# Kernel optimization log

Hardware: AMD Instinct MI355X
Metric: run time of the kernel (lower is better)

The kernel has to match this reference:

```python
import jax, jax.numpy as jnp
import numpy as np

NEG_SLOPE = 0.01  # torch nn.LeakyReLU default


def setup_inputs() -> dict:
    key = jax.random.key(0)
    k1, k2, k3 = jax.random.split(key, 3)
    B, H, D, L = 4, 8, 64, 2048
    q = jax.random.normal(k1, (B, H, D, L), dtype=jnp.float32)
    k = jax.random.normal(k2, (B, H, D, L), dtype=jnp.float32)
    v = jax.random.normal(k3, (B, H, D, L), dtype=jnp.float32)
    return {"q": q, "k": k, "v": v}


def reference(q, k, v):
    # q, k, v: [B, H, D, L] (note: feature dim BEFORE length, as in the torch module)
    d_tensor = q.shape[2]
    scale = 1.0 / np.sqrt(d_tensor).astype(np.float32)
    # scores = LeakyReLU(q^T k / sqrt(d)) : [B, H, Lq, Lk]
    scores = jnp.einsum('bhdq,bhdk->bhqk', q, k) * scale
    scores = jax.nn.leaky_relu(scores, negative_slope=NEG_SLOPE)
    psi = jax.nn.softmax(scores, axis=-1)
    # out = (psi @ v^T)^T : [B, H, D, Lq]
    out = jnp.einsum('bhqk,bhdk->bhdq', psi, v)
    return out
```

## Files before the change

kernel.cpp:

```cpp
#include <hip/hip_runtime.h>
#include <math.h>

#define DD 64
#define LL 2048
#define HEADS 32
#define TQ 128
#define TK 64
#define NTHREADS 512
#define QSCALE 0.18033688011112042f

typedef __bf16 bf16_t;
typedef __bf16 bf16x8 __attribute__((ext_vector_type(8)));
typedef float f32x16 __attribute__((ext_vector_type(16)));

__global__ __launch_bounds__(256)
void prep_bf16(const float* __restrict__ q, const float* __restrict__ k,
               const float* __restrict__ v, bf16_t* __restrict__ qt,
               bf16_t* __restrict__ kt, bf16_t* __restrict__ vb) {
  __shared__ float ld[64][65];
  const int t = threadIdx.x;
  const int which = blockIdx.z;
  const int head = blockIdx.y;
  const int l0 = blockIdx.x * 64;
  const size_t hoff = (size_t)head * DD * LL;
  if (which == 2) {
    const float* src = v + hoff;
    bf16_t* dst = vb + hoff;
    const int lp = (t & 31) * 2;
    const int db = (t >> 5) * 8;
    for (int i = 0; i < 8; ++i) {
      int d = db + i;
      float2 x = *(const float2*)(src + (size_t)d * LL + l0 + lp);
      union { bf16_t b[2]; unsigned u; } pk;
      pk.b[0] = (bf16_t)x.x;
      pk.b[1] = (bf16_t)x.y;
      *(unsigned*)(dst + (size_t)d * LL + l0 + lp) = pk.u;
    }
  } else {
    const float* src = (which == 0) ? (q + hoff) : (k + hoff);
    bf16_t* dst = (which == 0) ? (qt + hoff) : (kt + hoff);
    const float scale = (which == 0) ? QSCALE : 1.0f;
    const int l = t & 63;
    const int db = (t >> 6) * 16;
    for (int i = 0; i < 16; ++i) {
      int d = db + i;
      ld[l][d] = src[(size_t)d * LL + l0 + l] * scale;
    }
    __syncthreads();
    const int dp = (t & 31) * 2;
    const int lb = (t >> 5) * 8;
    for (int i = 0; i < 8; ++i) {
      int lw = lb + i;
      union { bf16_t b[2]; unsigned u; } pk;
      pk.b[0] = (bf16_t)ld[lw][dp];
      pk.b[1] = (bf16_t)ld[lw][dp + 1];
      *(unsigned*)(dst + (size_t)(l0 + lw) * DD + dp) = pk.u;
    }
  }
}

struct __align__(16) SMemA2 {
  bf16_t Qs[TQ][72];
  bf16_t Ks[2][TK][72];
  bf16_t Vs[2][DD][72];
};
union __align__(16) SMemU2 {
  SMemA2 a;
  float Oe[TQ][65];
};

__global__ __launch_bounds__(NTHREADS, 4)
void attn_flash_bf16_v2(const bf16_t* __restrict__ qt, const bf16_t* __restrict__ kt,
                        const bf16_t* __restrict__ vb, float* __restrict__ out) {
  __shared__ SMemU2 sm;
  __shared__ float rs1[TQ];
  const int tid  = threadIdx.x;
  const int w    = tid >> 6;
  const int lane = tid & 63;
  const int l31  = lane & 31;
  const int hh   = lane >> 5;
  const int strip = w & 3;
  const int half  = w >> 2;
  const int wbase = strip * 32;
  const int lkh   = half * 32;
  const int head = blockIdx.y;
  const int q0   = blockIdx.x * TQ;
  const size_t hoff = (size_t)head * DD * LL;
  const bf16_t* qp = qt + hoff;
  const bf16_t* kp = kt + hoff;
  const bf16_t* vp = vb + hoff;

  for (int g = 0; g < 2; ++g) {
    int c  = tid + NTHREADS * g;
    int lq = c >> 3;
    int d0 = (c & 7) * 8;
    bf16x8 x = *(const bf16x8*)(qp + (size_t)(q0 + lq) * DD + d0);
    *(bf16x8*)&sm.a.Qs[lq][d0] = x;
  }

  const int srow = tid >> 3;
  const int scol = (tid & 7) * 8;

  bf16x8 kreg = *(const bf16x8*)(kp + (size_t)srow * DD + scol);
  bf16x8 vreg = *(const bf16x8*)(vp + (size_t)srow * LL + scol);

  __syncthreads();
  bf16x8 bq[4];
  for (int kk = 0; kk < 4; ++kk)
    bq[kk] = *(const bf16x8*)&sm.a.Qs[wbase + l31][kk * 16 + 8 * hh];

  f32x16 oacc[2];
  for (int dt = 0; dt < 2; ++dt)
    for (int r = 0; r < 16; ++r) oacc[dt][r] = 0.f;
  float rsum = 0.f;

  for (int t = 0; t < LL / TK; ++t) {
    const int cur = t & 1;
    *(bf16x8*)&sm.a.Ks[cur][srow][scol] = kreg;
    *(bf16x8*)&sm.a.Vs[cur][srow][scol] = vreg;
    __syncthreads();

    if (t + 1 < LL / TK) {
      const int lk0n = (t + 1) * TK;
      kreg = *(const bf16x8*)(kp + (size_t)(lk0n + srow) * DD + scol);
      vreg = *(const bf16x8*)(vp + (size_t)srow * LL + lk0n + scol);
    }

    f32x16 st;
    for (int r = 0; r < 16; ++r) st[r] = 0.f;
    __builtin_amdgcn_s_setprio(1);
    for (int kk = 0; kk < 4; ++kk) {
      bf16x8 ak = *(const bf16x8*)&sm.a.Ks[cur][lkh + l31][kk * 16 + 8 * hh];
      st = __builtin_amdgcn_mfma_f32_32x32x16_bf16(ak, bq[kk], st, 0, 0, 0);
    }
    __builtin_amdgcn_s_setprio(0);

    unsigned pb[8];
    for (int r = 0; r < 16; ++r) {
      float s = st[r];
      s = fmaxf(s, 0.01f * s);
      float p = __builtin_amdgcn_exp2f(s);
      rsum += p;
      st[r] = p;
    }
    for (int qq = 0; qq < 8; ++qq) {
      union { bf16_t b[2]; unsigned u; } pk;
      pk.b[0] = (bf16_t)st[2 * qq];
      pk.b[1] = (bf16_t)st[2 * qq + 1];
      pb[qq] = pk.u;
    }

    for (int kk2 = 0; kk2 < 2; ++kk2) {
      unsigned l0 = pb[4 * kk2 + 0], l1 = pb[4 * kk2 + 1];
      unsigned l2 = pb[4 * kk2 + 2], l3 = pb[4 * kk2 + 3];
      unsigned s0 = hh ? l0 : l2;
      unsigned s1 = hh ? l1 : l3;
      unsigned f0 = (unsigned)__shfl_xor((int)s0, 32);
      unsigned f1 = (unsigned)__shfl_xor((int)s1, 32);
      union { unsigned u[4]; bf16x8 v; } ap;
      ap.u[0] = hh ? f0 : l0;
      ap.u[1] = hh ? f1 : l1;
      ap.u[2] = hh ? l2 : f0;
      ap.u[3] = hh ? l3 : f1;
      const int lkb = lkh + kk2 * 16 + 8 * hh;
      __builtin_amdgcn_s_setprio(1);
      for (int dt = 0; dt < 2; ++dt) {
        bf16x8 bv = *(const bf16x8*)&sm.a.Vs[cur][dt * 32 + l31][lkb];
        oacc[dt] = __builtin_amdgcn_mfma_f32_32x32x16_bf16(ap.v, bv, oacc[dt], 0, 0, 0);
      }
      __builtin_amdgcn_s_setprio(0);
    }
  }

  float rtot = rsum + __shfl_xor(rsum, 32);
  __syncthreads();
  if (half == 1) {
    rs1[wbase + l31] = rtot;
    for (int r = 0; r < 16; ++r) {
      int row = (r & 3) + 8 * (r >> 2) + 4 * hh;
      for (int dt = 0; dt < 2; ++dt)
        sm.Oe[wbase + row][dt * 32 + l31] = oacc[dt][r];
    }
  }
  __syncthreads();
  if (half == 0) {
    float tot = rtot + rs1[wbase + l31];
    rs1[wbase + l31] = 1.0f / tot;
    float inv[16];
    for (int r = 0; r < 16; ++r) {
      int row = (r & 3) + 8 * (r >> 2) + 4 * hh;
      inv[r] = rs1[wbase + row];
    }
    for (int r = 0; r < 16; ++r) {
      int row = (r & 3) + 8 * (r >> 2) + 4 * hh;
      for (int dt = 0; dt < 2; ++dt) {
        int col = dt * 32 + l31;
        sm.Oe[wbase + row][col] = (oacc[dt][r] + sm.Oe[wbase + row][col]) * inv[r];
      }
    }
  }
  __syncthreads();
  float* op = out + hoff + q0;
  for (int i = 0; i < 16; ++i) {
    int idx = tid + NTHREADS * i;
    int d   = idx >> 7;
    int lq  = idx & 127;
    op[(size_t)d * LL + lq] = sm.Oe[lq][d];
  }
}

struct __align__(16) SMemA {
  bf16_t Qs[TQ][72];
  bf16_t Ks[TK][72];
  bf16_t Vs[DD][72];
};
union __align__(16) SMemU {
  SMemA a;
  float Oe[TQ][65];
};

__global__ __launch_bounds__(NTHREADS, 4)
void attn_flash_bf16(const float* __restrict__ q, const float* __restrict__ k,
                     const float* __restrict__ v, float* __restrict__ out) {
  __shared__ SMemU sm;
  __shared__ float rs1[TQ];
  const int tid  = threadIdx.x;
  const int w    = tid >> 6;
  const int lane = tid & 63;
  const int l31  = lane & 31;
  const int hh   = lane >> 5;
  const int strip = w & 3;
  const int half  = w >> 2;
  const int wbase = strip * 32;
  const int lkh   = half * 32;
  const int head = blockIdx.y;
  const int q0   = blockIdx.x * TQ;
  const size_t hoff = (size_t)head * DD * LL;
  const float* qp = q + hoff;
  const float* kp = k + hoff;
  const float* vp = v + hoff;

  {
    int lq  = tid & 127;
    int d0q = (tid >> 7) * 16;
    const float* src = qp + q0 + lq;
    for (int g = 0; g < 2; ++g) {
      bf16x8 pk;
      for (int j = 0; j < 8; ++j)
        pk[j] = (bf16_t)(src[(size_t)(d0q + g * 8 + j) * LL] * QSCALE);
      *(bf16x8*)&sm.a.Qs[lq][d0q + g * 8] = pk;
    }
  }

  const int klk = tid & 63;
  const int kd0 = (tid >> 6) * 8;
  const int vd  = tid >> 3;
  const int vc8 = (tid & 7) * 8;

  float  kreg[8];
  float4 vreg[2];
  {
    const float* ks = kp + klk;
    for (int j = 0; j < 8; ++j) kreg[j] = ks[(size_t)(kd0 + j) * LL];
    vreg[0] = *(const float4*)(vp + (size_t)vd * LL + vc8);
    vreg[1] = *(const float4*)(vp + (size_t)vd * LL + vc8 + 4);
  }

  __syncthreads();
  bf16x8 bq[4];
  for (int kk = 0; kk < 4; ++kk)
    bq[kk] = *(const bf16x8*)&sm.a.Qs[wbase + l31][kk * 16 + 8 * hh];

  f32x16 oacc[2];
  for (int dt = 0; dt < 2; ++dt)
    for (int r = 0; r < 16; ++r) oacc[dt][r] = 0.f;
  float rsum = 0.f;

  for (int t = 0; t < LL / TK; ++t) {
    __syncthreads();
    {
      bf16x8 pk;
      for (int j = 0; j < 8; ++j) pk[j] = (bf16_t)kreg[j];
      *(bf16x8*)&sm.a.Ks[klk][kd0] = pk;
      bf16x8 pv;
      pv[0] = (bf16_t)vreg[0].x; pv[1] = (bf16_t)vreg[0].y;
      pv[2] = (bf16_t)vreg[0].z; pv[3] = (bf16_t)vreg[0].w;
      pv[4] = (bf16_t)vreg[1].x; pv[5] = (bf16_t)vreg[1].y;
      pv[6] = (bf16_t)vreg[1].z; pv[7] = (bf16_t)vreg[1].w;
      *(bf16x8*)&sm.a.Vs[vd][vc8] = pv;
    }
    __syncthreads();

    if (t + 1 < LL / TK) {
      const int lk0n = (t + 1) * TK;
      const float* ks = kp + lk0n + klk;
      for (int j = 0; j < 8; ++j) kreg[j] = ks[(size_t)(kd0 + j) * LL];
      vreg[0] = *(const float4*)(vp + (size_t)vd * LL + lk0n + vc8);
      vreg[1] = *(const float4*)(vp + (size_t)vd * LL + lk0n + vc8 + 4);
    }

    f32x16 st;
    for (int r = 0; r < 16; ++r) st[r] = 0.f;
    for (int kk = 0; kk < 4; ++kk) {
      bf16x8 ak = *(const bf16x8*)&sm.a.Ks[lkh + l31][kk * 16 + 8 * hh];
      st = __builtin_amdgcn_mfma_f32_32x32x16_bf16(ak, bq[kk], st, 0, 0, 0);
    }

    unsigned pb[8];
    for (int r = 0; r < 16; ++r) {
      float s = st[r];
      s = fmaxf(s, 0.01f * s);
      float p = __builtin_amdgcn_exp2f(s);
      rsum += p;
      st[r] = p;
    }
    for (int qq = 0; qq < 8; ++qq) {
      union { bf16_t b[2]; unsigned u; } pk;
      pk.b[0] = (bf16_t)st[2 * qq];
      pk.b[1] = (bf16_t)st[2 * qq + 1];
      pb[qq] = pk.u;
    }

    for (int kk2 = 0; kk2 < 2; ++kk2) {
      unsigned l0 = pb[4 * kk2 + 0], l1 = pb[4 * kk2 + 1];
      unsigned l2 = pb[4 * kk2 + 2], l3 = pb[4 * kk2 + 3];
      unsigned s0 = hh ? l0 : l2;
      unsigned s1 = hh ? l1 : l3;
      unsigned f0 = (unsigned)__shfl_xor((int)s0, 32);
      unsigned f1 = (unsigned)__shfl_xor((int)s1, 32);
      union { unsigned u[4]; bf16x8 v; } ap;
      ap.u[0] = hh ? f0 : l0;
      ap.u[1] = hh ? f1 : l1;
      ap.u[2] = hh ? l2 : f0;
      ap.u[3] = hh ? l3 : f1;
      const int lkb = lkh + kk2 * 16 + 8 * hh;
      for (int dt = 0; dt < 2; ++dt) {
        bf16x8 bv = *(const bf16x8*)&sm.a.Vs[dt * 32 + l31][lkb];
        oacc[dt] = __builtin_amdgcn_mfma_f32_32x32x16_bf16(ap.v, bv, oacc[dt], 0, 0, 0);
      }
    }
  }

  float rtot = rsum + __shfl_xor(rsum, 32);
  __syncthreads();
  if (half == 1) {
    rs1[wbase + l31] = rtot;
    for (int r = 0; r < 16; ++r) {
      int row = (r & 3) + 8 * (r >> 2) + 4 * hh;
      for (int dt = 0; dt < 2; ++dt)
        sm.Oe[wbase + row][dt * 32 + l31] = oacc[dt][r];
    }
  }
  __syncthreads();
  if (half == 0) {
    float tot = rtot + rs1[wbase + l31];
    rs1[wbase + l31] = 1.0f / tot;
    float inv[16];
    for (int r = 0; r < 16; ++r) {
      int row = (r & 3) + 8 * (r >> 2) + 4 * hh;
      inv[r] = rs1[wbase + row];
    }
    for (int r = 0; r < 16; ++r) {
      int row = (r & 3) + 8 * (r >> 2) + 4 * hh;
      for (int dt = 0; dt < 2; ++dt) {
        int col = dt * 32 + l31;
        sm.Oe[wbase + row][col] = (oacc[dt][r] + sm.Oe[wbase + row][col]) * inv[r];
      }
    }
  }
  __syncthreads();
  float* op = out + hoff + q0;
  for (int i = 0; i < 16; ++i) {
    int idx = tid + NTHREADS * i;
    int d   = idx >> 7;
    int lq  = idx & 127;
    op[(size_t)d * LL + lq] = sm.Oe[lq][d];
  }
}

extern "C" void kernel_launch(void* const* d_in, const int* in_sizes, int n_in,
                              void* d_out, int out_size, void* d_ws, size_t ws_size,
                              hipStream_t stream) {
  const float* q = (const float*)d_in[0];
  const float* k = (const float*)d_in[1];
  const float* v = (const float*)d_in[2];
  float* out = (float*)d_out;
  const size_t per_buf = (size_t)HEADS * DD * LL;
  const size_t need = 3 * per_buf * sizeof(bf16_t);
  if (d_ws && ws_size >= need) {
    bf16_t* qt = (bf16_t*)d_ws;
    bf16_t* kt = qt + per_buf;
    bf16_t* vb = kt + per_buf;
    prep_bf16<<<dim3(LL / 64, HEADS, 3), 256, 0, stream>>>(q, k, v, qt, kt, vb);
    attn_flash_bf16_v2<<<dim3(LL / TQ, HEADS), NTHREADS, 0, stream>>>(qt, kt, vb, out);
  } else {
    attn_flash_bf16<<<dim3(LL / TQ, HEADS), NTHREADS, 0, stream>>>(q, k, v, out);
  }
}
```

Before: 144.9 us.

## Halve query tile to 64 with 256 threads and fold Q conversion into attention kernel

The attention kernel now processes 64 query rows per block with 4 waves instead of 128 rows with 8 waves, which doubles the grid to 1024 blocks. Q is read as fp32, scaled and converted to bf16 inside the attention kernel, so the prep kernel only converts K and V. The Q tile shares LDS with the K double buffer, cutting shared memory per block so more blocks can be resident. The cost is that each K/V tile loaded from memory serves half as many queries, doubling K/V traffic per query. The in-kernel Q load is also strided and uncoalesced.

```diff
diff --git a/kernel.cpp b/kernel.cpp
--- a/kernel.cpp
+++ b/kernel.cpp
@@ -14,16 +14,15 @@
 typedef float f32x16 __attribute__((ext_vector_type(16)));
 
 __global__ __launch_bounds__(256)
-void prep_bf16(const float* __restrict__ q, const float* __restrict__ k,
-               const float* __restrict__ v, bf16_t* __restrict__ qt,
-               bf16_t* __restrict__ kt, bf16_t* __restrict__ vb) {
+void prep_bf16_kv(const float* __restrict__ k, const float* __restrict__ v,
+                  bf16_t* __restrict__ kt, bf16_t* __restrict__ vb) {
   __shared__ float ld[64][65];
   const int t = threadIdx.x;
   const int which = blockIdx.z;
   const int head = blockIdx.y;
   const int l0 = blockIdx.x * 64;
   const size_t hoff = (size_t)head * DD * LL;
-  if (which == 2) {
+  if (which == 1) {
     const float* src = v + hoff;
     bf16_t* dst = vb + hoff;
     const int lp = (t & 31) * 2;
@@ -37,14 +36,13 @@
       *(unsigned*)(dst + (size_t)d * LL + l0 + lp) = pk.u;
     }
   } else {
-    const float* src = (which == 0) ? (q + hoff) : (k + hoff);
-    bf16_t* dst = (which == 0) ? (qt + hoff) : (kt + hoff);
-    const float scale = (which == 0) ? QSCALE : 1.0f;
+    const float* src = k + hoff;
+    bf16_t* dst = kt + hoff;
     const int l = t & 63;
     const int db = (t >> 6) * 16;
     for (int i = 0; i < 16; ++i) {
       int d = db + i;
-      ld[l][d] = src[(size_t)d * LL + l0 + l] * scale;
+      ld[l][d] = src[(size_t)d * LL + l0 + l];
     }
     __syncthreads();
     const int dp = (t & 31) * 2;
@@ -59,55 +57,64 @@
   }
 }
 
-struct __align__(16) SMemA2 {
-  bf16_t Qs[TQ][72];
-  bf16_t Ks[2][TK][72];
-  bf16_t Vs[2][DD][72];
+struct __align__(16) SMemA3 {
+  union {
+    bf16_t Qs[64][72];
+    bf16_t Ks[2][64][72];
+  } qk;
+  bf16_t Vs[2][64][72];
 };
-union __align__(16) SMemU2 {
-  SMemA2 a;
-  float Oe[TQ][65];
+union __align__(16) SMemU3 {
+  SMemA3 a;
+  float Oe[64][65];
 };
 
-__global__ __launch_bounds__(NTHREADS, 4)
-void attn_flash_bf16_v2(const bf16_t* __restrict__ qt, const bf16_t* __restrict__ kt,
+__global__ __launch_bounds__(256, 4)
+void attn_flash_bf16_v3(const float* __restrict__ q, const bf16_t* __restrict__ kt,
                         const bf16_t* __restrict__ vb, float* __restrict__ out) {
-  __shared__ SMemU2 sm;
-  __shared__ float rs1[TQ];
+  __shared__ SMemU3 sm;
+  __shared__ float rs1[64];
   const int tid  = threadIdx.x;
   const int w    = tid >> 6;
   const int lane = tid & 63;
   const int l31  = lane & 31;
   const int hh   = lane >> 5;
-  const int strip = w & 3;
-  const int half  = w >> 2;
+  const int strip = w & 1;
+  const int half  = w >> 1;
   const int wbase = strip * 32;
   const int lkh   = half * 32;
   const int head = blockIdx.y;
-  const int q0   = blockIdx.x * TQ;
+  const int q0   = blockIdx.x * 64;
   const size_t hoff = (size_t)head * DD * LL;
-  const bf16_t* qp = qt + hoff;
+  const float*  qp = q  + hoff;
   const bf16_t* kp = kt + hoff;
   const bf16_t* vp = vb + hoff;
 
-  for (int g = 0; g < 2; ++g) {
-    int c  = tid + NTHREADS * g;
-    int lq = c >> 3;
-    int d0 = (c & 7) * 8;
-    bf16x8 x = *(const bf16x8*)(qp + (size_t)(q0 + lq) * DD + d0);
-    *(bf16x8*)&sm.a.Qs[lq][d0] = x;
-  }
-
-  const int srow = tid >> 3;
-  const int scol = (tid & 7) * 8;
-
-  bf16x8 kreg = *(const bf16x8*)(kp + (size_t)srow * DD + scol);
-  bf16x8 vreg = *(const bf16x8*)(vp + (size_t)srow * LL + scol);
+  {
+    int lq  = tid & 63;
+    int d0q = (tid >> 6) * 16;
+    const float* src = qp + q0 + lq;
+    for (int g = 0; g < 2; ++g) {
+      bf16x8 pk;
+      for (int j = 0; j < 8; ++j)
+        pk[j] = (bf16_t)(src[(size_t)(d0q + g * 8 + j) * LL] * QSCALE);
+      *(bf16x8*)&sm.a.qk.Qs[lq][d0q + g * 8] = pk;
+    }
+  }
+
+  const int srow = tid >> 2;
+  const int scol = (tid & 3) * 16;
+
+  bf16x8 kreg0 = *(const bf16x8*)(kp + (size_t)srow * DD + scol);
+  bf16x8 kreg1 = *(const bf16x8*)(kp + (size_t)srow * DD + scol + 8);
+  bf16x8 vreg0 = *(const bf16x8*)(vp + (size_t)srow * LL + scol);
+  bf16x8 vreg1 = *(const bf16x8*)(vp + (size_t)srow * LL + scol + 8);
 
   __syncthreads();
   bf16x8 bq[4];
   for (int kk = 0; kk < 4; ++kk)
-    bq[kk] = *(const bf16x8*)&sm.a.Qs[wbase + l31][kk * 16 + 8 * hh];
+    bq[kk] = *(const bf16x8*)&sm.a.qk.Qs[wbase + l31][kk * 16 + 8 * hh];
+  __syncthreads();
 
   f32x16 oacc[2];
   for (int dt = 0; dt < 2; ++dt)
@@ -116,21 +123,25 @@
 
   for (int t = 0; t < LL / TK; ++t) {
     const int cur = t & 1;
-    *(bf16x8*)&sm.a.Ks[cur][srow][scol] = kreg;
-    *(bf16x8*)&sm.a.Vs[cur][srow][scol] = vreg;
+    *(bf16x8*)&sm.a.qk.Ks[cur][srow][scol]     = kreg0;
+    *(bf16x8*)&sm.a.qk.Ks[cur][srow][scol + 8] = kreg1;
+    *(bf16x8*)&sm.a.Vs[cur][srow][scol]        = vreg0;
+    *(bf16x8*)&sm.a.Vs[cur][srow][scol + 8]    = vreg1;
     __syncthreads();
 
     if (t + 1 < LL / TK) {
       const int lk0n = (t + 1) * TK;
-      kreg = *(const bf16x8*)(kp + (size_t)(lk0n + srow) * DD + scol);
-      vreg = *(const bf16x8*)(vp + (size_t)srow * LL + lk0n + scol);
+      kreg0 = *(const bf16x8*)(kp + (size_t)(lk0n + srow) * DD + scol);
+      kreg1 = *(const bf16x8*)(kp + (size_t)(lk0n + srow) * DD + scol + 8);
+      vreg0 = *(const bf16x8*)(vp + (size_t)srow * LL + lk0n + scol);
+      vreg1 = *(const bf16x8*)(vp + (size_t)srow * LL + lk0n + scol + 8);
     }
 
     f32x16 st;
     for (int r = 0; r < 16; ++r) st[r] = 0.f;
     __builtin_amdgcn_s_setprio(1);
     for (int kk = 0; kk < 4; ++kk) {
-      bf16x8 ak = *(const bf16x8*)&sm.a.Ks[cur][lkh + l31][kk * 16 + 8 * hh];
+      bf16x8 ak = *(const bf16x8*)&sm.a.qk.Ks[cur][lkh + l31][kk * 16 + 8 * hh];
       st = __builtin_amdgcn_mfma_f32_32x32x16_bf16(ak, bq[kk], st, 0, 0, 0);
     }
     __builtin_amdgcn_s_setprio(0);
@@ -202,9 +213,9 @@
   __syncthreads();
   float* op = out + hoff + q0;
   for (int i = 0; i < 16; ++i) {
-    int idx = tid + NTHREADS * i;
-    int d   = idx >> 7;
-    int lq  = idx & 127;
+    int idx = tid + 256 * i;
+    int d   = idx >> 6;
+    int lq  = idx & 63;
     op[(size_t)d * LL + lq] = sm.Oe[lq][d];
   }
 }
@@ -386,13 +397,12 @@
   const float* v = (const float*)d_in[2];
   float* out = (float*)d_out;
   const size_t per_buf = (size_t)HEADS * DD * LL;
-  const size_t need = 3 * per_buf * sizeof(bf16_t);
+  const size_t need = 2 * per_buf * sizeof(bf16_t);
   if (d_ws && ws_size >= need) {
-    bf16_t* qt = (bf16_t*)d_ws;
-    bf16_t* kt = qt + per_buf;
+    bf16_t* kt = (bf16_t*)d_ws;
     bf16_t* vb = kt + per_buf;
-    prep_bf16<<<dim3(LL / 64, HEADS, 3), 256, 0, stream>>>(q, k, v, qt, kt, vb);
-    attn_flash_bf16_v2<<<dim3(LL / TQ, HEADS), NTHREADS, 0, stream>>>(qt, kt, vb, out);
+    prep_bf16_kv<<<dim3(LL / 64, HEADS, 2), 256, 0, stream>>>(k, v, kt, vb);
+    attn_flash_bf16_v3<<<dim3(LL / 64, HEADS), 256, 0, stream>>>(q, kt, vb, out);
   } else {
     attn_flash_bf16<<<dim3(LL / TQ, HEADS), NTHREADS, 0, stream>>>(q, k, v, out);
   }
```

Result: slower. 148.5 us (+2.4%).

## Fuse Q conversion into attention kernel, alias Q/K smem, swizzle block order

Applied to the files above, without the earlier changes.

Removes the Q prep pass, so the attention kernel now reads fp32 Q directly and converts it to bf16 in shared memory. Q storage is overlapped with the K double buffer, which shrinks LDS per block and allows more blocks per CU (launch bounds raised to 8); an extra barrier is added to make the reuse safe. Block indices are remapped over a 1D grid so that consecutive blocks fall in different heads, and the row sum is split into four accumulators to shorten the dependency chain. The extra occupancy may cost registers, and the strided fp32 Q load inside the main kernel is less coalesced.

```diff
diff --git a/kernel.cpp b/kernel.cpp
--- a/kernel.cpp
+++ b/kernel.cpp
@@ -14,16 +14,15 @@
 typedef float f32x16 __attribute__((ext_vector_type(16)));
 
 __global__ __launch_bounds__(256)
-void prep_bf16(const float* __restrict__ q, const float* __restrict__ k,
-               const float* __restrict__ v, bf16_t* __restrict__ qt,
-               bf16_t* __restrict__ kt, bf16_t* __restrict__ vb) {
+void prep_bf16_kv(const float* __restrict__ k, const float* __restrict__ v,
+                  bf16_t* __restrict__ kt, bf16_t* __restrict__ vb) {
   __shared__ float ld[64][65];
   const int t = threadIdx.x;
   const int which = blockIdx.z;
   const int head = blockIdx.y;
   const int l0 = blockIdx.x * 64;
   const size_t hoff = (size_t)head * DD * LL;
-  if (which == 2) {
+  if (which == 1) {
     const float* src = v + hoff;
     bf16_t* dst = vb + hoff;
     const int lp = (t & 31) * 2;
@@ -37,14 +36,13 @@
       *(unsigned*)(dst + (size_t)d * LL + l0 + lp) = pk.u;
     }
   } else {
-    const float* src = (which == 0) ? (q + hoff) : (k + hoff);
-    bf16_t* dst = (which == 0) ? (qt + hoff) : (kt + hoff);
-    const float scale = (which == 0) ? QSCALE : 1.0f;
+    const float* src = k + hoff;
+    bf16_t* dst = kt + hoff;
     const int l = t & 63;
     const int db = (t >> 6) * 16;
     for (int i = 0; i < 16; ++i) {
       int d = db + i;
-      ld[l][d] = src[(size_t)d * LL + l0 + l] * scale;
+      ld[l][d] = src[(size_t)d * LL + l0 + l];
     }
     __syncthreads();
     const int dp = (t & 31) * 2;
@@ -59,20 +57,22 @@
   }
 }
 
-struct __align__(16) SMemA2 {
-  bf16_t Qs[TQ][72];
-  bf16_t Ks[2][TK][72];
+struct __align__(16) SMemA4 {
+  union {
+    bf16_t Qs[TQ][72];
+    bf16_t Ks[2][TK][72];
+  } qk;
   bf16_t Vs[2][DD][72];
 };
-union __align__(16) SMemU2 {
-  SMemA2 a;
+union __align__(16) SMemU4 {
+  SMemA4 a;
   float Oe[TQ][65];
 };
 
-__global__ __launch_bounds__(NTHREADS, 4)
-void attn_flash_bf16_v2(const bf16_t* __restrict__ qt, const bf16_t* __restrict__ kt,
+__global__ __launch_bounds__(NTHREADS, 8)
+void attn_flash_bf16_v4(const float* __restrict__ q, const bf16_t* __restrict__ kt,
                         const bf16_t* __restrict__ vb, float* __restrict__ out) {
-  __shared__ SMemU2 sm;
+  __shared__ SMemU4 sm;
   __shared__ float rs1[TQ];
   const int tid  = threadIdx.x;
   const int w    = tid >> 6;
@@ -83,41 +83,49 @@
   const int half  = w >> 2;
   const int wbase = strip * 32;
   const int lkh   = half * 32;
-  const int head = blockIdx.y;
-  const int q0   = blockIdx.x * TQ;
+  const int bid  = blockIdx.x;
+  const int j    = bid >> 3;
+  const int head = (bid & 7) + 8 * (j >> 4);
+  const int q0   = (j & 15) * TQ;
   const size_t hoff = (size_t)head * DD * LL;
-  const bf16_t* qp = qt + hoff;
+  const float*  qp = q  + hoff;
   const bf16_t* kp = kt + hoff;
   const bf16_t* vp = vb + hoff;
 
-  for (int g = 0; g < 2; ++g) {
-    int c  = tid + NTHREADS * g;
-    int lq = c >> 3;
-    int d0 = (c & 7) * 8;
-    bf16x8 x = *(const bf16x8*)(qp + (size_t)(q0 + lq) * DD + d0);
-    *(bf16x8*)&sm.a.Qs[lq][d0] = x;
-  }
-
   const int srow = tid >> 3;
   const int scol = (tid & 7) * 8;
 
   bf16x8 kreg = *(const bf16x8*)(kp + (size_t)srow * DD + scol);
   bf16x8 vreg = *(const bf16x8*)(vp + (size_t)srow * LL + scol);
 
+  {
+    int lq  = tid & 127;
+    int d0q = (tid >> 7) * 16;
+    const float* src = qp + q0 + lq;
+    for (int g = 0; g < 2; ++g) {
+      bf16x8 pk;
+      for (int jj = 0; jj < 8; ++jj)
+        pk[jj] = (bf16_t)(src[(size_t)(d0q + g * 8 + jj) * LL] * QSCALE);
+      *(bf16x8*)&sm.a.qk.Qs[lq][d0q + g * 8] = pk;
+    }
+  }
+
   __syncthreads();
   bf16x8 bq[4];
   for (int kk = 0; kk < 4; ++kk)
-    bq[kk] = *(const bf16x8*)&sm.a.Qs[wbase + l31][kk * 16 + 8 * hh];
+    bq[kk] = *(const bf16x8*)&sm.a.qk.Qs[wbase + l31][kk * 16 + 8 * hh];
+  __syncthreads();
 
   f32x16 oacc[2];
   for (int dt = 0; dt < 2; ++dt)
     for (int r = 0; r < 16; ++r) oacc[dt][r] = 0.f;
-  float rsum = 0.f;
+  float rsl[4];
+  for (int i = 0; i < 4; ++i) rsl[i] = 0.f;
 
   for (int t = 0; t < LL / TK; ++t) {
     const int cur = t & 1;
-    *(bf16x8*)&sm.a.Ks[cur][srow][scol] = kreg;
-    *(bf16x8*)&sm.a.Vs[cur][srow][scol] = vreg;
+    *(bf16x8*)&sm.a.qk.Ks[cur][srow][scol] = kreg;
+    *(bf16x8*)&sm.a.Vs[cur][srow][scol]    = vreg;
     __syncthreads();
 
     if (t + 1 < LL / TK) {
@@ -130,17 +138,18 @@
     for (int r = 0; r < 16; ++r) st[r] = 0.f;
     __builtin_amdgcn_s_setprio(1);
     for (int kk = 0; kk < 4; ++kk) {
-      bf16x8 ak = *(const bf16x8*)&sm.a.Ks[cur][lkh + l31][kk * 16 + 8 * hh];
+      bf16x8 ak = *(const bf16x8*)&sm.a.qk.Ks[cur][lkh + l31][kk * 16 + 8 * hh];
       st = __builtin_amdgcn_mfma_f32_32x32x16_bf16(ak, bq[kk], st, 0, 0, 0);
     }
     __builtin_amdgcn_s_setprio(0);
 
     unsigned pb[8];
+#pragma unroll
     for (int r = 0; r < 16; ++r) {
       float s = st[r];
       s = fmaxf(s, 0.01f * s);
       float p = __builtin_amdgcn_exp2f(s);
-      rsum += p;
+      rsl[r & 3] += p;
       st[r] = p;
     }
     for (int qq = 0; qq < 8; ++qq) {
@@ -172,6 +181,7 @@
     }
   }
 
+  float rsum = (rsl[0] + rsl[1]) + (rsl[2] + rsl[3]);
   float rtot = rsum + __shfl_xor(rsum, 32);
   __syncthreads();
   if (half == 1) {
@@ -246,8 +256,8 @@
     const float* src = qp + q0 + lq;
     for (int g = 0; g < 2; ++g) {
       bf16x8 pk;
-      for (int j = 0; j < 8; ++j)
-        pk[j] = (bf16_t)(src[(size_t)(d0q + g * 8 + j) * LL] * QSCALE);
+      for (int jj = 0; jj < 8; ++jj)
+        pk[jj] = (bf16_t)(src[(size_t)(d0q + g * 8 + jj) * LL] * QSCALE);
       *(bf16x8*)&sm.a.Qs[lq][d0q + g * 8] = pk;
     }
   }
@@ -261,7 +271,7 @@
   float4 vreg[2];
   {
     const float* ks = kp + klk;
-    for (int j = 0; j < 8; ++j) kreg[j] = ks[(size_t)(kd0 + j) * LL];
+    for (int jj = 0; jj < 8; ++jj) kreg[jj] = ks[(size_t)(kd0 + jj) * LL];
     vreg[0] = *(const float4*)(vp + (size_t)vd * LL + vc8);
     vreg[1] = *(const float4*)(vp + (size_t)vd * LL + vc8 + 4);
   }
@@ -280,7 +290,7 @@
     __syncthreads();
     {
       bf16x8 pk;
-      for (int j = 0; j < 8; ++j) pk[j] = (bf16_t)kreg[j];
+      for (int jj = 0; jj < 8; ++jj) pk[jj] = (bf16_t)kreg[jj];
       *(bf16x8*)&sm.a.Ks[klk][kd0] = pk;
       bf16x8 pv;
       pv[0] = (bf16_t)vreg[0].x; pv[1] = (bf16_t)vreg[0].y;
@@ -294,7 +304,7 @@
     if (t + 1 < LL / TK) {
       const int lk0n = (t + 1) * TK;
       const float* ks = kp + lk0n + klk;
-      for (int j = 0; j < 8; ++j) kreg[j] = ks[(size_t)(kd0 + j) * LL];
+      for (int jj = 0; jj < 8; ++jj) kreg[jj] = ks[(size_t)(kd0 + jj) * LL];
       vreg[0] = *(const float4*)(vp + (size_t)vd * LL + lk0n + vc8);
       vreg[1] = *(const float4*)(vp + (size_t)vd * LL + lk0n + vc8 + 4);
     }
@@ -386,13 +396,12 @@
   const float* v = (const float*)d_in[2];
   float* out = (float*)d_out;
   const size_t per_buf = (size_t)HEADS * DD * LL;
-  const size_t need = 3 * per_buf * sizeof(bf16_t);
+  const size_t need = 2 * per_buf * sizeof(bf16_t);
   if (d_ws && ws_size >= need) {
-    bf16_t* qt = (bf16_t*)d_ws;
-    bf16_t* kt = qt + per_buf;
+    bf16_t* kt = (bf16_t*)d_ws;
     bf16_t* vb = kt + per_buf;
-    prep_bf16<<<dim3(LL / 64, HEADS, 3), 256, 0, stream>>>(q, k, v, qt, kt, vb);
-    attn_flash_bf16_v2<<<dim3(LL / TQ, HEADS), NTHREADS, 0, stream>>>(qt, kt, vb, out);
+    prep_bf16_kv<<<dim3(LL / 64, HEADS, 2), 256, 0, stream>>>(k, v, kt, vb);
+    attn_flash_bf16_v4<<<dim3((LL / TQ) * HEADS), NTHREADS, 0, stream>>>(q, kt, vb, out);
   } else {
     attn_flash_bf16<<<dim3(LL / TQ, HEADS), NTHREADS, 0, stream>>>(q, k, v, out);
   }
```

Measured after the change: 453.8 us. +213.1%, slower.
